# Kernel tuning notes

Hardware: AMD Instinct MI355X
Metric: run time of the kernel (lower is better)

## Reference

```python
import jax, jax.numpy as jnp
import numpy as np

NUM_CLASSES = 1000
SCALE = 1.0

def setup_inputs() -> dict:
    key = jax.random.key(0)
    x = jax.random.normal(key, (32768, NUM_CLASSES), dtype=jnp.float32)
    return {"input": x}

def reference(input) -> jnp.ndarray:
    # residual defaults to input in the torch module
    r = input                                   # [B, C]
    n = NUM_CLASSES
    ra = jnp.abs(r)
    mean = jnp.mean(ra, axis=-1, keepdims=True)
    std = jnp.std(ra, axis=-1, keepdims=True, ddof=1)  # torch.std is unbiased
    w = SCALE * jax.nn.sigmoid((ra - mean) / std)       # [B, C]
    # W = I + 1/(n-1) * diag(w) @ (ones - n*I);  (W r)_i = r_i + w_i/(n-1)*(sum(r) - n*r_i)
    s = jnp.sum(r, axis=-1, keepdims=True)              # [B, 1]
    out = r + w / (n - 1) * (s - n * r)
    return out
```

## Files before the change

kernel.cpp:

```cpp
#include <hip/hip_runtime.h>
#include <math.h>

#define NC 1000
#define NV 250

__device__ __forceinline__ float sigmoidf(float x) {
    return 1.0f / (1.0f + expf(-x));
}

__global__ __launch_bounds__(256)
void smooth_filter_kernel(const float* __restrict__ in, float* __restrict__ out) {
    const int row  = blockIdx.x;
    const int t    = threadIdx.x;
    const int wave = t >> 6;
    const int lane = t & 63;

    const float4* __restrict__ rp = (const float4*)(in + (size_t)row * NC);

    float4 v = make_float4(0.f, 0.f, 0.f, 0.f);
    if (t < NV) v = rp[t];

    const float a0 = fabsf(v.x), a1 = fabsf(v.y), a2 = fabsf(v.z), a3 = fabsf(v.w);

    float s_r  = (v.x + v.y) + (v.z + v.w);
    float s_a  = (a0 + a1) + (a2 + a3);
    float s_a2 = (a0 * a0 + a1 * a1) + (a2 * a2 + a3 * a3);

    #pragma unroll
    for (int off = 32; off > 0; off >>= 1) {
        s_r  += __shfl_down(s_r,  off, 64);
        s_a  += __shfl_down(s_a,  off, 64);
        s_a2 += __shfl_down(s_a2, off, 64);
    }

    __shared__ float red[3][4];
    if (lane == 0) {
        red[0][wave] = s_r;
        red[1][wave] = s_a;
        red[2][wave] = s_a2;
    }
    __syncthreads();

    const float S   = (red[0][0] + red[0][1]) + (red[0][2] + red[0][3]);
    const float SA  = (red[1][0] + red[1][1]) + (red[1][2] + red[1][3]);
    const float SA2 = (red[2][0] + red[2][1]) + (red[2][2] + red[2][3]);

    const float mean    = SA * (1.0f / NC);
    const float var     = (SA2 - (float)NC * mean * mean) * (1.0f / (NC - 1));
    const float inv_std = rsqrtf(var);
    const float c       = 1.0f / (NC - 1);

    if (t < NV) {
        float4 o;
        o.x = v.x + sigmoidf((a0 - mean) * inv_std) * c * (S - (float)NC * v.x);
        o.y = v.y + sigmoidf((a1 - mean) * inv_std) * c * (S - (float)NC * v.y);
        o.z = v.z + sigmoidf((a2 - mean) * inv_std) * c * (S - (float)NC * v.z);
        o.w = v.w + sigmoidf((a3 - mean) * inv_std) * c * (S - (float)NC * v.w);
        ((float4*)(out + (size_t)row * NC))[t] = o;
    }
}

extern "C" void kernel_launch(void* const* d_in, const int* in_sizes, int n_in,
                              void* d_out, int out_size, void* d_ws, size_t ws_size,
                              hipStream_t stream) {
    const float* in  = (const float*)d_in[0];
    float*       out = (float*)d_out;
    const int rows   = in_sizes[0] / NC;
    smooth_filter_kernel<<<rows, 256, 0, stream>>>(in, out);
}
```

Measured before the change: 216.8 us.

## Map one wavefront per row, drop shared-memory reduction, use fast exp/rcp and nontemporal stores

```diff
diff --git a/kernel.cpp b/kernel.cpp
--- a/kernel.cpp
+++ b/kernel.cpp
@@ -1,62 +1,92 @@
 #include <hip/hip_runtime.h>
 #include <math.h>
 
-#define NC 1000
-#define NV 250
+#define NC   1000
+#define NVEC 250
+#define WPB  4
+#define L2E  1.4426950408889634f
 
-__device__ __forceinline__ float sigmoidf(float x) {
-    return 1.0f / (1.0f + expf(-x));
-}
+typedef float v4f __attribute__((ext_vector_type(4)));
+
+#if __has_builtin(__builtin_amdgcn_exp2f)
+#define FAST_EXP2(x) __builtin_amdgcn_exp2f(x)
+#else
+#define FAST_EXP2(x) exp2f(x)
+#endif
+
+#if __has_builtin(__builtin_amdgcn_rcpf)
+#define FAST_RCP(x) __builtin_amdgcn_rcpf(x)
+#else
+#define FAST_RCP(x) (1.0f / (x))
+#endif
 
 __global__ __launch_bounds__(256)
-void smooth_filter_kernel(const float* __restrict__ in, float* __restrict__ out) {
-    const int row  = blockIdx.x;
-    const int t    = threadIdx.x;
-    const int wave = t >> 6;
-    const int lane = t & 63;
+void smooth_filter_kernel(const float* __restrict__ in,
+                          float* __restrict__ out,
+                          int rows) {
+    const int lane = threadIdx.x & 63;
+    const int row  = blockIdx.x * WPB + (threadIdx.x >> 6);
+    if (row >= rows) return;
 
-    const float4* __restrict__ rp = (const float4*)(in + (size_t)row * NC);
+    const float4* __restrict__ rp = (const float4*)(in  + (size_t)row * NC);
+    v4f*          __restrict__ op = (v4f*)         (out + (size_t)row * NC);
 
-    float4 v = make_float4(0.f, 0.f, 0.f, 0.f);
-    if (t < NV) v = rp[t];
+    float4 v[4];
+    v[3] = make_float4(0.f, 0.f, 0.f, 0.f);
+    v[0] = rp[lane];
+    v[1] = rp[lane + 64];
+    v[2] = rp[lane + 128];
+    const bool tail = (lane < (NVEC - 192));
+    if (tail) v[3] = rp[lane + 192];
 
-    const float a0 = fabsf(v.x), a1 = fabsf(v.y), a2 = fabsf(v.z), a3 = fabsf(v.w);
-
-    float s_r  = (v.x + v.y) + (v.z + v.w);
-    float s_a  = (a0 + a1) + (a2 + a3);
-    float s_a2 = (a0 * a0 + a1 * a1) + (a2 * a2 + a3 * a3);
+    float s_r = 0.f, s_a = 0.f, s_a2 = 0.f;
+    #pragma unroll
+    for (int k = 0; k < 4; ++k) {
+        const float a0 = fabsf(v[k].x), a1 = fabsf(v[k].y);
+        const float a2 = fabsf(v[k].z), a3 = fabsf(v[k].w);
+        s_r  += (v[k].x + v[k].y) + (v[k].z + v[k].w);
+        s_a  += (a0 + a1) + (a2 + a3);
+        s_a2 += (a0 * a0 + a1 * a1) + (a2 * a2 + a3 * a3);
+    }
 
     #pragma unroll
     for (int off = 32; off > 0; off >>= 1) {
-        s_r  += __shfl_down(s_r,  off, 64);
-        s_a  += __shfl_down(s_a,  off, 64);
-        s_a2 += __shfl_down(s_a2, off, 64);
+        s_r  += __shfl_xor(s_r,  off, 64);
+        s_a  += __shfl_xor(s_a,  off, 64);
+        s_a2 += __shfl_xor(s_a2, off, 64);
     }
 
-    __shared__ float red[3][4];
-    if (lane == 0) {
-        red[0][wave] = s_r;
-        red[1][wave] = s_a;
-        red[2][wave] = s_a2;
-    }
-    __syncthreads();
+    const float mean    = s_a * (1.0f / NC);
+    const float var     = (s_a2 - (float)NC * mean * mean) * (1.0f / (NC - 1));
+    const float inv_std = rsqrtf(var);
 
-    const float S   = (red[0][0] + red[0][1]) + (red[0][2] + red[0][3]);
-    const float SA  = (red[1][0] + red[1][1]) + (red[1][2] + red[1][3]);
-    const float SA2 = (red[2][0] + red[2][1]) + (red[2][2] + red[2][3]);
+    const float kx = -inv_std * L2E;
+    const float bx =  mean * inv_std * L2E;
+    const float c  = 1.0f / (NC - 1);
+    const float cS = c * s_r;
+    const float cn = c * (float)NC;
 
-    const float mean    = SA * (1.0f / NC);
-    const float var     = (SA2 - (float)NC * mean * mean) * (1.0f / (NC - 1));
-    const float inv_std = rsqrtf(var);
-    const float c       = 1.0f / (NC - 1);
-
-    if (t < NV) {
-        float4 o;
-        o.x = v.x + sigmoidf((a0 - mean) * inv_std) * c * (S - (float)NC * v.x);
-        o.y = v.y + sigmoidf((a1 - mean) * inv_std) * c * (S - (float)NC * v.y);
-        o.z = v.z + sigmoidf((a2 - mean) * inv_std) * c * (S - (float)NC * v.z);
-        o.w = v.w + sigmoidf((a3 - mean) * inv_std) * c * (S - (float)NC * v.w);
-        ((float4*)(out + (size_t)row * NC))[t] = o;
+    #pragma unroll
+    for (int k = 0; k < 4; ++k) {
+        if (k == 3 && !tail) break;
+        v4f o;
+        {
+            const float e = FAST_EXP2(fmaf(fabsf(v[k].x), kx, bx));
+            o.x = fmaf(FAST_RCP(1.0f + e), fmaf(-cn, v[k].x, cS), v[k].x);
+        }
+        {
+            const float e = FAST_EXP2(fmaf(fabsf(v[k].y), kx, bx));
+            o.y = fmaf(FAST_RCP(1.0f + e), fmaf(-cn, v[k].y, cS), v[k].y);
+        }
+        {
+            const float e = FAST_EXP2(fmaf(fabsf(v[k].z), kx, bx));
+            o.z = fmaf(FAST_RCP(1.0f + e), fmaf(-cn, v[k].z, cS), v[k].z);
+        }
+        {
+            const float e = FAST_EXP2(fmaf(fabsf(v[k].w), kx, bx));
+            o.w = fmaf(FAST_RCP(1.0f + e), fmaf(-cn, v[k].w, cS), v[k].w);
+        }
+        __builtin_nontemporal_store(o, &op[lane + 64 * k]);
     }
 }
 
@@ -66,5 +96,6 @@
     const float* in  = (const float*)d_in[0];
     float*       out = (float*)d_out;
     const int rows   = in_sizes[0] / NC;
-    smooth_filter_kernel<<<rows, 256, 0, stream>>>(in, out);
+    const int blocks = (rows + WPB - 1) / WPB;
+    smooth_filter_kernel<<<blocks, 256, 0, stream>>>(in, out, rows);
 }
```

After: 227.2 us. +4.8%, slower.
